# Kernel optimization log

Measured on AMD Instinct MI355X. Metric: run time of the kernel, lower is better.

The kernel has to match this reference:

```python
import jax, jax.numpy as jnp
import numpy as np

B, N, INIT_DIM, DIMS, K, RADIUS = 8, 4096, 6, 64, 32, 0.1
EPS = 1e-5


def layer_norm(x, g, b):
    m = jnp.mean(x, axis=-1, keepdims=True)
    v = jnp.mean((x - m) ** 2, axis=-1, keepdims=True)
    return (x - m) * jax.lax.rsqrt(v + EPS) * g + b


def query_ball(sqrdists, radius, k):
    # sqrdists: [B, S, N] squared distances. PointNet++ ball query:
    # indices outside the ball -> N, sort, take first k, backfill with first idx.
    n = sqrdists.shape[-1]
    idx = jnp.arange(n, dtype=jnp.int32)
    gi = jnp.where(sqrdists <= radius * radius, idx[None, None, :], n)
    gi = jnp.sort(gi, axis=-1)[..., :k]
    first = gi[..., :1]
    return jnp.where(gi == n, first, gi)  # [B, S, k]


def setup_inputs() -> dict:
    key = jax.random.key(0)
    ks = jax.random.split(key, 10)
    inputs = jax.random.normal(ks[0], (B, N, INIT_DIM), dtype=jnp.float32)
    coordinates = jax.random.uniform(ks[1], (B, N, 3), dtype=jnp.float32)
    # squared pairwise distances via |a|^2 + |b|^2 - 2 a.b (avoids [B,N,N,3] temp)
    sq = jnp.sum(coordinates ** 2, axis=-1)
    distance_matrices = (sq[:, :, None] + sq[:, None, :]
                         - 2.0 * jnp.einsum('bnc,bmc->bnm', coordinates, coordinates))
    distance_matrices = jnp.maximum(distance_matrices, 0.0)
    s1 = 1.0 / np.sqrt(INIT_DIM)
    s2 = 1.0 / np.sqrt(2 * DIMS)
    W1 = jax.random.uniform(ks[2], (INIT_DIM, DIMS), minval=-s1, maxval=s1)
    b1 = jax.random.uniform(ks[3], (DIMS,), minval=-s1, maxval=s1)
    g1 = jnp.ones((DIMS,), jnp.float32)
    be1 = jnp.zeros((DIMS,), jnp.float32)
    W2 = jax.random.uniform(ks[4], (2 * DIMS, DIMS), minval=-s2, maxval=s2)
    b2 = jax.random.uniform(ks[5], (DIMS,), minval=-s2, maxval=s2)
    g2 = jnp.ones((DIMS,), jnp.float32)
    be2 = jnp.zeros((DIMS,), jnp.float32)
    return {"inputs": inputs, "coordinates": coordinates,
            "distance_matrices": distance_matrices,
            "W1": W1, "b1": b1, "g1": g1, "be1": be1,
            "W2": W2, "b2": b2, "g2": g2, "be2": be2}


def reference(inputs, coordinates, distance_matrices, W1, b1, g1, be1, W2, b2, g2, be2):
    # embedding: Linear -> LayerNorm -> ReLU
    x = jax.nn.relu(layer_norm(inputs @ W1 + b1, g1, be1))  # [B,N,D]
    idx = query_ball(distance_matrices, RADIUS, K)           # [B,N,K] int32
    ball = jax.vmap(lambda xb, ib: xb[ib])(x, idx)           # [B,N,K,D]
    xc = x[:, :, None, :]                                    # [B,N,1,D]
    rel = ball - xc
    comb = jnp.concatenate([rel, jnp.broadcast_to(xc, rel.shape)], axis=-1)  # [B,N,K,2D]
    y = jax.nn.relu(layer_norm(comb @ W2 + b2, g2, be2))     # [B,N,K,D]
    return jnp.max(y, axis=-2)                               # [B,N,D]
```

## Files before the change

### kernel.cpp

```cpp
#include <hip/hip_runtime.h>
#include <cstdint>
#include <cstddef>

#define BB 8
#define NN 4096
#define IDIM 6
#define DIMS 64
#define KNB 32
#define BN (BB * NN)
#define NCELL 1024

static constexpr float LN_EPS = 1e-5f;
static constexpr float INV_SIDE = 1.0f / 0.11f;

template<int CTRL>
__device__ __forceinline__ float dpp_xadd(float v) {
    int r = __builtin_amdgcn_update_dpp(0, __float_as_int(v), CTRL, 0xF, 0xF, true);
    return v + __int_as_float(r);
}
template<int OFFS>
__device__ __forceinline__ float swz_xadd(float v) {
    int r = __builtin_amdgcn_ds_swizzle(__float_as_int(v), OFFS);
    return v + __int_as_float(r);
}
__device__ __forceinline__ float wsum64(float v) {
    v = dpp_xadd<0xB1>(v);
    v = dpp_xadd<0x4E>(v);
    v = swz_xadd<0x101F>(v);
    v = dpp_xadd<0x128>(v);
    v = swz_xadd<0x401F>(v);
    v += __shfl_xor(v, 32, 64);
    return v;
}

template<int K, int J>
__device__ __forceinline__ void bstep(int& v, int lane) {
    const int o = __shfl_xor(v, J, 64);
    const bool up = (lane & K) == 0;
    const bool lower = (lane & J) == 0;
    v = (lower == up) ? min(v, o) : max(v, o);
}
__device__ __forceinline__ void sort64(int& v, int lane) {
    bstep<2,1>(v,lane);
    bstep<4,2>(v,lane);  bstep<4,1>(v,lane);
    bstep<8,4>(v,lane);  bstep<8,2>(v,lane);  bstep<8,1>(v,lane);
    bstep<16,8>(v,lane); bstep<16,4>(v,lane); bstep<16,2>(v,lane); bstep<16,1>(v,lane);
    bstep<32,16>(v,lane); bstep<32,8>(v,lane); bstep<32,4>(v,lane); bstep<32,2>(v,lane); bstep<32,1>(v,lane);
    bstep<64,32>(v,lane); bstep<64,16>(v,lane); bstep<64,8>(v,lane); bstep<64,4>(v,lane); bstep<64,2>(v,lane); bstep<64,1>(v,lane);
}

__device__ __forceinline__ int cell_of(float x, float y, float z) {
    const int cx = min((int)(x * INV_SIDE), 9);
    const int cy = min((int)(y * INV_SIDE), 9);
    const int cz = min((int)(z * INV_SIDE), 9);
    return cx * 100 + cy * 10 + cz;
}

__global__ __launch_bounds__(256) void k_count(const float* __restrict__ coords,
                                               int* __restrict__ counts,
                                               float4* __restrict__ cq)
{
    const int p = blockIdx.x * 256 + threadIdx.x;
    const float x = coords[3 * p], y = coords[3 * p + 1], z = coords[3 * p + 2];
    cq[p] = make_float4(x, y, z, fmaf(z, z, fmaf(y, y, x * x)));
    const int b = p >> 12;
    atomicAdd(&counts[(b << 10) + cell_of(x, y, z)], 1);
}

__global__ __launch_bounds__(256) void k_scan(const int* __restrict__ counts,
                                              int* __restrict__ starts,
                                              int* __restrict__ cursor)
{
    __shared__ int ssum[256];
    const int b = blockIdx.x, t = threadIdx.x;
    const int base = (b << 10) + (t << 2);
    const int c0 = counts[base], c1 = counts[base + 1];
    const int c2 = counts[base + 2], c3 = counts[base + 3];
    const int s = c0 + c1 + c2 + c3;
    ssum[t] = s;
    __syncthreads();
    int acc = s;
    for (int off = 1; off < 256; off <<= 1) {
        const int v = (t >= off) ? ssum[t - off] : 0;
        __syncthreads();
        acc += v; ssum[t] = acc;
        __syncthreads();
    }
    int run = acc - s;
    starts[base] = run; cursor[base] = run; run += c0;
    starts[base + 1] = run; cursor[base + 1] = run; run += c1;
    starts[base + 2] = run; cursor[base + 2] = run; run += c2;
    starts[base + 3] = run; cursor[base + 3] = run;
}

__global__ __launch_bounds__(256) void k_scatter(const float* __restrict__ coords,
                                                 int* __restrict__ cursor,
                                                 int* __restrict__ csr)
{
    const int p = blockIdx.x * 256 + threadIdx.x;
    const float x = coords[3 * p], y = coords[3 * p + 1], z = coords[3 * p + 2];
    const int b = p >> 12;
    const int pos = atomicAdd(&cursor[(b << 10) + cell_of(x, y, z)], 1);
    csr[(b << 12) + pos] = p & (NN - 1);
}

__global__ __launch_bounds__(256, 4) void k1_feat(
    const float* __restrict__ inp, const float* __restrict__ W1,
    const float* __restrict__ b1, const float* __restrict__ g1,
    const float* __restrict__ be1, const float* __restrict__ W2,
    const float* __restrict__ b2,
    float* __restrict__ a_buf, float* __restrict__ c_buf,
    float* __restrict__ Sa_buf)
{
    const int lane = threadIdx.x & 63;
    const int p = (blockIdx.x << 2) + (threadIdx.x >> 6);
    const float* ip = inp + (size_t)p * IDIM;
    float h = b1[lane];
#pragma unroll
    for (int j = 0; j < IDIM; ++j)
        h = fmaf(ip[j], W1[j * DIMS + lane], h);
    const float mean = wsum64(h) * (1.0f / DIMS);
    const float dv = h - mean;
    const float var = wsum64(dv * dv) * (1.0f / DIMS);
    const float x = fmaxf(dv * rsqrtf(var + LN_EPS) * g1[lane] + be1[lane], 0.0f);

    float a = 0.0f, cp = 0.0f;
    const int xi = __float_as_int(x);
#pragma unroll 8
    for (int j = 0; j < DIMS; ++j) {
        const int sj = __builtin_amdgcn_readlane(xi, j);
        if (sj != 0) {
            const float xj = __int_as_float(sj);
            a  = fmaf(xj, W2[j * DIMS + lane], a);
            cp = fmaf(xj, W2[(DIMS + j) * DIMS + lane], cp);
        }
    }
    const float c = cp + b2[lane] - a;
    a_buf[(size_t)p * DIMS + lane] = a;
    c_buf[(size_t)p * DIMS + lane] = c;
    const float sa = wsum64(a);
    if (lane == 0) Sa_buf[p] = sa;
}

__global__ __launch_bounds__(512, 4) void k23(
    const float4* __restrict__ cq, const float* __restrict__ DM,
    const float* __restrict__ a_buf, const float* __restrict__ c_buf,
    const float* __restrict__ Sa_buf, const int* __restrict__ starts,
    const int* __restrict__ counts, const int* __restrict__ csr,
    const float* __restrict__ g2, const float* __restrict__ be2,
    float* __restrict__ outp)
{
    __shared__ int p_tab[8][32];
    __shared__ int s_tab[8][32];
    __shared__ int hits[8][64];

    const int bid = ((blockIdx.x & 7) << 9) + (blockIdx.x >> 3);
    const int lane = threadIdx.x & 63;
    const int w = threadIdx.x >> 6;
    const int row = (bid << 3) + w;
    const int b = row >> 12;
    const int n = row & (NN - 1);

    const float4* __restrict__ cqb = cq + ((size_t)b << 12);
    const float4 pn = cqb[n];
    const float R2 = (float)(0.1 * 0.1);
    const float thr = R2 - pn.w;
    const float BAND = 1e-4f;
    const float* __restrict__ dmrow = DM + (size_t)row * NN;

    const int cx = min((int)(pn.x * INV_SIDE), 9);
    const int cy = min((int)(pn.y * INV_SIDE), 9);
    const int cz = min((int)(pn.z * INV_SIDE), 9);

    int cnt_i = 0, start_i = 0;
    if (lane < 27) {
        const int dx = lane / 9 - 1, dy = (lane / 3) % 3 - 1, dz = lane % 3 - 1;
        const int X = cx + dx, Y = cy + dy, Z = cz + dz;
        if ((unsigned)X <= 9u && (unsigned)Y <= 9u && (unsigned)Z <= 9u) {
            const int cid = (b << 10) + X * 100 + Y * 10 + Z;
            cnt_i = counts[cid];
            start_i = starts[cid];
        }
    }
    int incl = cnt_i;
#pragma unroll
    for (int s = 1; s < 64; s <<= 1) {
        const int tv = __shfl_up(incl, s, 64);
        if (lane >= s) incl += tv;
    }
    const int T = __builtin_amdgcn_readlane(incl, 63);
    if (lane < 32) {
        p_tab[w][lane] = (lane < 27) ? (incl - cnt_i) : T;
        s_tab[w][lane] = start_i;
    }
    __syncthreads();

    int cnt = 0;
    for (int tb = 0; tb < T; tb += 64) {
        const int t = tb + lane;
        int mm = 0;
        bool within = false;
        if (t < T) {
            int c = 0;
#pragma unroll
            for (int s = 16; s >= 1; s >>= 1)
                if (p_tab[w][c + s] <= t) c += s;
            const int j = t - p_tab[w][c];
            mm = csr[(b << 12) + s_tab[w][c] + j];
            const float4 pm = cqb[mm];
            const float dot = fmaf(pn.z, pm.z, fmaf(pn.y, pm.y, pn.x * pm.x));
            const float e = fmaf(-2.0f, dot, pm.w);
            within = (e <= thr);
            if (fabsf(e - thr) <= BAND) within = (dmrow[mm] <= R2);
        }
        const unsigned long long msk = __ballot(within);
        if (within) {
            const int pos = cnt + __popcll(msk & ((1ull << lane) - 1ull));
            if (pos < 64) hits[w][pos] = mm;
        }
        cnt += __popcll(msk);
    }
    __syncthreads();

    int myidx = 0x7fffffff;
    if (cnt <= 64) {
        if (lane < cnt) myidx = hits[w][lane];
    } else {
        cnt = 0;
        for (int mb = 0; mb < NN && cnt < KNB; mb += 64) {
            const int mmf = mb + lane;
            const float4 pm = cqb[mmf];
            const float dot = fmaf(pn.z, pm.z, fmaf(pn.y, pm.y, pn.x * pm.x));
            const float e = fmaf(-2.0f, dot, pm.w);
            bool wi = (e <= thr);
            if (fabsf(e - thr) <= BAND) wi = (dmrow[mmf] <= R2);
            unsigned long long m2 = __ballot(wi);
            while (m2 && cnt < KNB) {
                const int src = (int)__builtin_ctzll(m2);
                if (lane == cnt) myidx = mb + src;
                m2 &= m2 - 1;
                ++cnt;
            }
        }
    }
    sort64(myidx, lane);
    const int KK = min(cnt, KNB);

    const float cv = c_buf[(size_t)row * DIMS + lane];
    const float Sc = wsum64(cv);
    const float gg = g2[lane], bb = be2[lane];
    const float* __restrict__ abase = a_buf + ((size_t)(b << 12) * DIMS);
    const float* __restrict__ Sab = Sa_buf + (b << 12);
    const int mix = myidx;

    float om0 = 0.0f, om1 = 0.0f, om2 = 0.0f, om3 = 0.0f;
    for (int k = 0; k < KK; k += 4) {
        const int ka = min(k + 1, KK - 1);
        const int kb2 = min(k + 2, KK - 1);
        const int kc = min(k + 3, KK - 1);
        const int m0 = __builtin_amdgcn_readlane(mix, k);
        const int m1 = __builtin_amdgcn_readlane(mix, ka);
        const int m2 = __builtin_amdgcn_readlane(mix, kb2);
        const int m3 = __builtin_amdgcn_readlane(mix, kc);
        const float mu0 = (Sab[m0] + Sc) * (1.0f / DIMS);
        const float mu1 = (Sab[m1] + Sc) * (1.0f / DIMS);
        const float mu2 = (Sab[m2] + Sc) * (1.0f / DIMS);
        const float mu3 = (Sab[m3] + Sc) * (1.0f / DIMS);
        const float d0 = abase[(size_t)m0 * DIMS + lane] + cv - mu0;
        const float d1 = abase[(size_t)m1 * DIMS + lane] + cv - mu1;
        const float d2 = abase[(size_t)m2 * DIMS + lane] + cv - mu2;
        const float d3 = abase[(size_t)m3 * DIMS + lane] + cv - mu3;
        const float q0 = wsum64(d0 * d0);
        const float q1 = wsum64(d1 * d1);
        const float q2 = wsum64(d2 * d2);
        const float q3 = wsum64(d3 * d3);
        const float y0 = d0 * rsqrtf(q0 * (1.0f / DIMS) + LN_EPS) * gg + bb;
        const float y1 = d1 * rsqrtf(q1 * (1.0f / DIMS) + LN_EPS) * gg + bb;
        const float y2 = d2 * rsqrtf(q2 * (1.0f / DIMS) + LN_EPS) * gg + bb;
        const float y3 = d3 * rsqrtf(q3 * (1.0f / DIMS) + LN_EPS) * gg + bb;
        om0 = fmaxf(om0, y0);
        om1 = fmaxf(om1, y1);
        om2 = fmaxf(om2, y2);
        om3 = fmaxf(om3, y3);
    }
    outp[(size_t)row * DIMS + lane] =
        fmaxf(fmaxf(fmaxf(om0, om1), fmaxf(om2, om3)), 0.0f);
}

extern "C" void kernel_launch(void* const* d_in, const int* in_sizes, int n_in,
                              void* d_out, int out_size, void* d_ws, size_t ws_size,
                              hipStream_t stream)
{
    const float* inp    = (const float*)d_in[0];
    const float* coords = (const float*)d_in[1];
    const float* DM     = (const float*)d_in[2];
    const float* W1     = (const float*)d_in[3];
    const float* b1v    = (const float*)d_in[4];
    const float* g1     = (const float*)d_in[5];
    const float* be1    = (const float*)d_in[6];
    const float* W2     = (const float*)d_in[7];
    const float* b2v    = (const float*)d_in[8];
    const float* g2     = (const float*)d_in[9];
    const float* be2    = (const float*)d_in[10];
    float* out = (float*)d_out;

    char* ws = (char*)d_ws;
    size_t off = 0;
    float*  a_buf  = (float*)(ws + off); off += (size_t)BN * DIMS * 4;
    float*  c_buf  = (float*)(ws + off); off += (size_t)BN * DIMS * 4;
    float*  Sa_buf = (float*)(ws + off); off += (size_t)BN * 4;
    float4* cq     = (float4*)(ws + off); off += (size_t)BN * 16;
    int*    counts = (int*)(ws + off); off += (size_t)BB * NCELL * 4;
    int*    starts = (int*)(ws + off); off += (size_t)BB * NCELL * 4;
    int*    cursor = (int*)(ws + off); off += (size_t)BB * NCELL * 4;
    int*    csr    = (int*)(ws + off); off += (size_t)BN * 4;

    hipMemsetAsync(counts, 0, (size_t)BB * NCELL * 4, stream);
    k_count<<<dim3(BN / 256), dim3(256), 0, stream>>>(coords, counts, cq);
    k_scan<<<dim3(BB), dim3(256), 0, stream>>>(counts, starts, cursor);
    k_scatter<<<dim3(BN / 256), dim3(256), 0, stream>>>(coords, cursor, csr);
    k1_feat<<<dim3(BN / 4), dim3(256), 0, stream>>>(
        inp, W1, b1v, g1, be1, W2, b2v, a_buf, c_buf, Sa_buf);
    k23<<<dim3(BN / 8), dim3(512), 0, stream>>>(
        cq, DM, a_buf, c_buf, Sa_buf, starts, counts, csr, g2, be2, out);
}
```

Baseline: 685.8 us.

## Fuse grid count, scan and scatter into one per-batch shared-memory kernel

```diff
diff --git a/kernel.cpp b/kernel.cpp
--- a/kernel.cpp
+++ b/kernel.cpp
@@ -56,52 +56,51 @@
     return cx * 100 + cy * 10 + cz;
 }
 
-__global__ __launch_bounds__(256) void k_count(const float* __restrict__ coords,
-                                               int* __restrict__ counts,
-                                               float4* __restrict__ cq)
+__global__ __launch_bounds__(1024) void k_csr(const float* __restrict__ coords,
+                                              float4* __restrict__ cq,
+                                              int* __restrict__ counts_g,
+                                              int* __restrict__ starts_g,
+                                              int* __restrict__ csr)
 {
-    const int p = blockIdx.x * 256 + threadIdx.x;
-    const float x = coords[3 * p], y = coords[3 * p + 1], z = coords[3 * p + 2];
-    cq[p] = make_float4(x, y, z, fmaf(z, z, fmaf(y, y, x * x)));
-    const int b = p >> 12;
-    atomicAdd(&counts[(b << 10) + cell_of(x, y, z)], 1);
-}
-
-__global__ __launch_bounds__(256) void k_scan(const int* __restrict__ counts,
-                                              int* __restrict__ starts,
-                                              int* __restrict__ cursor)
-{
-    __shared__ int ssum[256];
-    const int b = blockIdx.x, t = threadIdx.x;
-    const int base = (b << 10) + (t << 2);
-    const int c0 = counts[base], c1 = counts[base + 1];
-    const int c2 = counts[base + 2], c3 = counts[base + 3];
-    const int s = c0 + c1 + c2 + c3;
-    ssum[t] = s;
-    __syncthreads();
-    int acc = s;
-    for (int off = 1; off < 256; off <<= 1) {
-        const int v = (t >= off) ? ssum[t - off] : 0;
+    __shared__ int cnt_s[NCELL];
+    __shared__ int cur_s[NCELL];
+    const int b = blockIdx.x;
+    const int t = threadIdx.x;
+    cnt_s[t] = 0;
+    __syncthreads();
+
+    int mycell[4];
+#pragma unroll
+    for (int i = 0; i < 4; ++i) {
+        const int pl = (i << 10) + t;
+        const int p = (b << 12) + pl;
+        const float x = coords[3 * p], y = coords[3 * p + 1], z = coords[3 * p + 2];
+        cq[p] = make_float4(x, y, z, fmaf(z, z, fmaf(y, y, x * x)));
+        mycell[i] = cell_of(x, y, z);
+        atomicAdd(&cnt_s[mycell[i]], 1);
+    }
+    __syncthreads();
+
+    const int count = cnt_s[t];
+    int acc = count;
+    for (int off = 1; off < NCELL; off <<= 1) {
+        const int u = (t >= off) ? cnt_s[t - off] : 0;
         __syncthreads();
-        acc += v; ssum[t] = acc;
+        acc += u; cnt_s[t] = acc;
         __syncthreads();
     }
-    int run = acc - s;
-    starts[base] = run; cursor[base] = run; run += c0;
-    starts[base + 1] = run; cursor[base + 1] = run; run += c1;
-    starts[base + 2] = run; cursor[base + 2] = run; run += c2;
-    starts[base + 3] = run; cursor[base + 3] = run;
-}
-
-__global__ __launch_bounds__(256) void k_scatter(const float* __restrict__ coords,
-                                                 int* __restrict__ cursor,
-                                                 int* __restrict__ csr)
-{
-    const int p = blockIdx.x * 256 + threadIdx.x;
-    const float x = coords[3 * p], y = coords[3 * p + 1], z = coords[3 * p + 2];
-    const int b = p >> 12;
-    const int pos = atomicAdd(&cursor[(b << 10) + cell_of(x, y, z)], 1);
-    csr[(b << 12) + pos] = p & (NN - 1);
+    const int start = acc - count;
+    counts_g[(b << 10) + t] = count;
+    starts_g[(b << 10) + t] = start;
+    cur_s[t] = start;
+    __syncthreads();
+
+#pragma unroll
+    for (int i = 0; i < 4; ++i) {
+        const int pl = (i << 10) + t;
+        const int pos = atomicAdd(&cur_s[mycell[i]], 1);
+        csr[(b << 12) + pos] = pl;
+    }
 }
 
 __global__ __launch_bounds__(256, 4) void k1_feat(
@@ -113,7 +112,7 @@
     float* __restrict__ Sa_buf)
 {
     const int lane = threadIdx.x & 63;
-    const int p = (blockIdx.x << 2) + (threadIdx.x >> 6);
+    const int p = __builtin_amdgcn_readfirstlane((blockIdx.x << 2) + (threadIdx.x >> 6));
     const float* ip = inp + (size_t)p * IDIM;
     float h = b1[lane];
 #pragma unroll
@@ -312,13 +311,9 @@
     float4* cq     = (float4*)(ws + off); off += (size_t)BN * 16;
     int*    counts = (int*)(ws + off); off += (size_t)BB * NCELL * 4;
     int*    starts = (int*)(ws + off); off += (size_t)BB * NCELL * 4;
-    int*    cursor = (int*)(ws + off); off += (size_t)BB * NCELL * 4;
     int*    csr    = (int*)(ws + off); off += (size_t)BN * 4;
 
-    hipMemsetAsync(counts, 0, (size_t)BB * NCELL * 4, stream);
-    k_count<<<dim3(BN / 256), dim3(256), 0, stream>>>(coords, counts, cq);
-    k_scan<<<dim3(BB), dim3(256), 0, stream>>>(counts, starts, cursor);
-    k_scatter<<<dim3(BN / 256), dim3(256), 0, stream>>>(coords, cursor, csr);
+    k_csr<<<dim3(BB), dim3(1024), 0, stream>>>(coords, cq, counts, starts, csr);
     k1_feat<<<dim3(BN / 4), dim3(256), 0, stream>>>(
         inp, W1, b1v, g1, be1, W2, b2v, a_buf, c_buf, Sa_buf);
     k23<<<dim3(BN / 8), dim3(512), 0, stream>>>(
```

Result: no change. 673.4 us (-1.8%).
